# Kernel tuning notes

Measured on AMD Instinct MI355X. Metric: run time of the kernel, lower is better.

Reference implementation:

```python
import jax, jax.numpy as jnp
import numpy as np

B, N, FOV = 64, 128, 9
CH = [3, 32, 64, 128]
FLAT = CH[-1] * FOV * FOV  # 10368
ENC = 128
K = 3
G1, G2 = 128, 128
A = 5
EPS = 1e-5


def setup_inputs() -> dict:
    key = jax.random.key(0)
    ks = jax.random.split(key, 24)
    d = {}
    d["states"] = jax.random.normal(ks[0], (B, N, 3, FOV, FOV), jnp.float32)
    d["gso"] = jax.random.uniform(ks[1], (B, N, N), jnp.float32)
    i = 2
    for l in range(3):
        cin, cout = CH[l], CH[l + 1]
        d[f"c{l+1}_w"] = jax.random.normal(ks[i], (cout, cin, 3, 3), jnp.float32) * 0.05; i += 1
        d[f"c{l+1}_b"] = jnp.zeros((cout,), jnp.float32)
        d[f"c{l+1}_g"] = jnp.ones((cout,), jnp.float32)
        d[f"c{l+1}_be"] = jnp.zeros((cout,), jnp.float32)
    d["enc_w"] = jax.random.normal(ks[i], (ENC, FLAT), jnp.float32) * (1.0 / np.sqrt(FLAT)); i += 1
    d["enc_b"] = jnp.zeros((ENC,), jnp.float32)
    d["g1_w"] = jax.random.normal(ks[i], (K, G1, ENC), jnp.float32) * (1.0 / np.sqrt(ENC * K)); i += 1
    d["g1_b"] = jnp.zeros((G1,), jnp.float32)
    d["g2_w"] = jax.random.normal(ks[i], (K, G2, G1), jnp.float32) * (1.0 / np.sqrt(G1 * K)); i += 1
    d["g2_b"] = jnp.zeros((G2,), jnp.float32)
    d["act_w"] = jax.random.normal(ks[i], (A, G2), jnp.float32) * (1.0 / np.sqrt(G2)); i += 1
    d["act_b"] = jnp.zeros((A,), jnp.float32)
    return d


def _conv_bn_relu(x, w, b, gamma, beta):
    # 3x3, stride 1, padding 1 -> SAME; NCHW/OIHW
    y = jax.lax.conv_general_dilated(
        x, w, window_strides=(1, 1), padding="SAME",
        dimension_numbers=("NCHW", "OIHW", "NCHW"))
    y = y + b[None, :, None, None]
    # BatchNorm2d in training mode: batch statistics over (N, H, W)
    mu = jnp.mean(y, axis=(0, 2, 3), keepdims=True)
    var = jnp.var(y, axis=(0, 2, 3), keepdims=True)
    y = (y - mu) * jax.lax.rsqrt(var + EPS)
    y = y * gamma[None, :, None, None] + beta[None, :, None, None]
    return jax.nn.relu(y)


def _graph_filter(x, S, w, b):
    # x: [B, F, N], S: [B, N, N], w: [K, G, F] -> y = sum_k W_k (x S^k) + b
    out = jnp.einsum("bfn,gf->bgn", x, w[0])
    xk = x
    for k in range(1, w.shape[0]):
        xk = jnp.einsum("bfn,bnm->bfm", xk, S)
        out = out + jnp.einsum("bfn,gf->bgn", xk, w[k])
    return out + b[None, :, None]


def reference(states, gso,
              c1_w, c1_b, c1_g, c1_be,
              c2_w, c2_b, c2_g, c2_be,
              c3_w, c3_b, c3_g, c3_be,
              enc_w, enc_b, g1_w, g1_b, g2_w, g2_b, act_w, act_b):
    x = states.reshape(B * N, 3, FOV, FOV)
    x = _conv_bn_relu(x, c1_w, c1_b, c1_g, c1_be)
    x = _conv_bn_relu(x, c2_w, c2_b, c2_g, c2_be)
    x = _conv_bn_relu(x, c3_w, c3_b, c3_g, c3_be)
    x = x.reshape(B * N, FLAT)
    x = x @ enc_w.T + enc_b                    # [B*N, ENC]
    x = x.reshape(B, N, ENC).transpose(0, 2, 1)  # [B, F, N]
    x = jax.nn.relu(_graph_filter(x, gso, g1_w, g1_b))
    x = jax.nn.relu(_graph_filter(x, gso, g2_w, g2_b))
    x = x.transpose(0, 2, 1).reshape(B * N, G2)
    logits = x @ act_w.T + act_b
    return logits.reshape(B, N, A)
```

## Files before the change

### kernel.cpp

```cpp
#include <hip/hip_runtime.h>
#include <hip/hip_bf16.h>
#include <stdint.h>


#define NIMG 8192
#define NPIX 81
#define FLAT 10368

typedef __hip_bfloat16 bf16;
typedef short bf16x8 __attribute__((ext_vector_type(8)));
typedef float f32x4 __attribute__((ext_vector_type(4)));

__device__ __forceinline__ float bflo(unsigned u) { return __uint_as_float(u << 16); }
__device__ __forceinline__ float bfhi(unsigned u) { return __uint_as_float(u & 0xffff0000u); }
__device__ __forceinline__ unsigned short f2bf(float f) {
    unsigned u = __float_as_uint(f);
    return (unsigned short)((u + 0x7fff + ((u >> 16) & 1)) >> 16);
}

__device__ __forceinline__ bf16x8 bn8(bf16x8 a, const float* sc, const float* sh) {
    union U { bf16x8 v; unsigned u[4]; } in, out;
    in.v = a;
#pragma unroll
    for (int d = 0; d < 4; d++) {
        float lo = fmaxf(fmaf(bflo(in.u[d]), sc[2 * d],     sh[2 * d]),     0.f);
        float hi = fmaxf(fmaf(bfhi(in.u[d]), sc[2 * d + 1], sh[2 * d + 1]), 0.f);
        out.u[d] = (unsigned)f2bf(lo) | ((unsigned)f2bf(hi) << 16);
    }
    return out.v;
}

__global__ void fill_sentinel(float* __restrict__ out, int n) {
    int i = blockIdx.x * 256 + threadIdx.x;
    if (i < n) out[i] = 1.0e9f;
}

__global__ void prep_w(const float* __restrict__ c1w, const float* __restrict__ c2w,
                       const float* __restrict__ c3w,
                       float* __restrict__ w1t, bf16* __restrict__ w2m,
                       bf16* __restrict__ w3m) {
    int i0 = blockIdx.x * blockDim.x + threadIdx.x;
    int stride = gridDim.x * blockDim.x;
    for (int i = i0; i < 27 * 32; i += stride) w1t[i] = c1w[(i & 31) * 27 + (i >> 5)];
    for (int i = i0; i < 64 * 288; i += stride) {
        int oc = i / 288, r = i - oc * 288, t = r >> 5, ci = r & 31;
        w2m[i] = __float2bfloat16(c2w[oc * 288 + ci * 9 + t]);
    }
    for (int i = i0; i < 128 * 576; i += stride) {
        int oc = i / 576, r = i - oc * 576, t = r >> 6, ci = r & 63;
        w3m[i] = __float2bfloat16(c3w[oc * 576 + ci * 9 + t]);
    }
}

__global__ void prep_enc(const float* __restrict__ encw, bf16* __restrict__ ewb) {
    int i0 = blockIdx.x * blockDim.x + threadIdx.x;
    int stride = gridDim.x * blockDim.x;
    for (int i = i0; i < 128 * FLAT; i += stride) {
        int e = i / FLAT, r = i - e * FLAT;
        int kk = r >> 5, c32 = r & 31;
        int px = kk >> 2, cc = kk & 3;
        ewb[i] = __float2bfloat16(encw[(size_t)e * FLAT + (cc * 32 + c32) * 81 + px]);
    }
}

__device__ __forceinline__ void load_row(const float* __restrict__ p, float* r) {
    float4 a = *(const float4*)p;
    float4 b = *(const float4*)(p + 4);
    float4 c = *(const float4*)(p + 8);
    r[0]=a.x; r[1]=a.y; r[2]=a.z;  r[3]=a.w;
    r[4]=b.x; r[5]=b.y; r[6]=b.z;  r[7]=b.w;
    r[8]=c.x; r[9]=c.y; r[10]=c.z; r[11]=c.w;
}

__device__ __forceinline__ void conv_body(const float* __restrict__ inp,
                                          const float* __restrict__ wv, float* acc) {
    float rb[3][12];
    load_row(inp, rb[0]);
    load_row(inp + 12, rb[1]);
#pragma unroll
    for (int oy = 0; oy < 9; oy++) {
        load_row(inp + (oy + 2) * 12, rb[(oy + 2) % 3]);
#pragma unroll
        for (int ky = 0; ky < 3; ky++) {
            const float* r = rb[(oy + ky) % 3];
#pragma unroll
            for (int ox = 0; ox < 9; ox++) {
                float s = acc[oy * 9 + ox];
                s = fmaf(r[ox + 0], wv[ky * 3 + 0], s);
                s = fmaf(r[ox + 1], wv[ky * 3 + 1], s);
                s = fmaf(r[ox + 2], wv[ky * 3 + 2], s);
                acc[oy * 9 + ox] = s;
            }
        }
    }
}

__global__ __launch_bounds__(128) void conv1_kernel(const float* __restrict__ xin,
        const float* __restrict__ wt, const float* __restrict__ bias,
        bf16* __restrict__ xout, float* __restrict__ sacc) {
    __shared__ __align__(16) float lds[4 * 3 * 132];
    __shared__ float Sl[128], Ql[128];
    int t = threadIdx.x;
    int img0 = blockIdx.x * 4;
    for (int i = t; i < 4 * 3 * 132; i += 128) lds[i] = 0.f;
    __syncthreads();
    const float* src = xin + (size_t)img0 * 243;
    for (int i = t; i < 4 * 243; i += 128) {
        int il = i / 243, rem = i - il * 243;
        int ci = rem / 81, px = rem - ci * 81;
        lds[(il * 3 + ci) * 132 + (px / 9 + 1) * 12 + (px % 9) + 1] = src[i];
    }
    __syncthreads();
    int oc = t & 31, il = t >> 5;
    const float* base = lds + il * 3 * 132;
    float acc[81];
    float bb = bias[oc];
#pragma unroll
    for (int i = 0; i < 81; i++) acc[i] = bb;
#pragma unroll
    for (int ci = 0; ci < 3; ci++) {
        float wv[9];
#pragma unroll
        for (int k = 0; k < 9; k++) wv[k] = wt[(ci * 9 + k) * 32 + oc];
        conv_body(base + ci * 132, wv, acc);
    }
    bf16* dst = xout + (size_t)(img0 + il) * 32 + oc;
    const size_t PXS = (size_t)NIMG * 32;
    float s = 0.f, q = 0.f;
#pragma unroll
    for (int p = 0; p < 81; p++) {
        float v = acc[p];
        s += v; q = fmaf(v, v, q);
        dst[p * PXS] = __float2bfloat16(v);
    }
    Sl[il * 32 + oc] = s;
    Ql[il * 32 + oc] = q;
    __syncthreads();
    if (t < 32)
        atomicAdd(&sacc[t], Sl[t] + Sl[32 + t] + Sl[64 + t] + Sl[96 + t]);
    else if (t < 64) {
        int c = t - 32;
        atomicAdd(&sacc[32 + c], Ql[c] + Ql[32 + c] + Ql[64 + c] + Ql[96 + c]);
    }
}

template <int CI, int COT, int OCS>
__global__ __launch_bounds__(256, 2) void conv_tile(const bf16* __restrict__ xin,
        const bf16* __restrict__ wm, const float* __restrict__ bias,
        const float* __restrict__ st, bf16* __restrict__ xout,
        float* __restrict__ sacc) {
    constexpr int NCH = CI / 32;
    constexpr int NCHO = COT / 32;
    constexpr int ROW = 9 * CI;
    constexpr int STEPS = 9 * NCH;
    constexpr int PHASES = STEPS / 9;
    constexpr int HS = STEPS / PHASES;
    constexpr size_t CSTRIDE = (size_t)NIMG * 32;
    __shared__ bf16 Bs[HS * 4 * 64 * 8];
    __shared__ float Ss[2][4][64];

    const int lin = blockIdx.x;
    const int xcd = lin & 7;
    const int slot = lin >> 3;
    constexpr int PSL = 81 * OCS;
    const int igl = slot / PSL;
    const int rem = slot - igl * PSL;
    const int p = rem / OCS;
    const int ob = rem - p * OCS;
    const int ig = xcd * 4 + igl;
    const int oc0 = ob * 64;
    const int py = p / 9, pxx = p - py * 9;
    const int tid = threadIdx.x;
    const int lane = tid & 63, wv = tid >> 6;
    const int m = lane & 15, quad = lane >> 4;
    const long img0 = (long)ig * 256 + wv * 64;

    int qt[9]; bool vt[9];
#pragma unroll
    for (int t = 0; t < 9; t++) {
        int iy = py + t / 3 - 1, ix = pxx + (t % 3) - 1;
        vt[t] = ((unsigned)iy < 9u) && ((unsigned)ix < 9u);
        qt[t] = vt[t] ? iy * 9 + ix : p;
    }

    float scv[NCH][8], shv[NCH][8];
#pragma unroll
    for (int ch = 0; ch < NCH; ch++)
#pragma unroll
        for (int j = 0; j < 8; j++) {
            int ci = ch * 32 + quad * 8 + j;
            scv[ch][j] = st[ci];
            shv[ch][j] = st[CI + ci];
        }

    f32x4 acc[4][4];
#pragma unroll
    for (int nf = 0; nf < 4; nf++) {
        float bb = bias[oc0 + nf * 16 + m];
#pragma unroll
        for (int ms = 0; ms < 4; ms++) {
            acc[ms][nf][0] = bb; acc[ms][nf][1] = bb;
            acc[ms][nf][2] = bb; acc[ms][nf][3] = bb;
        }
    }
    const bf16* ab[4];
#pragma unroll
    for (int ms = 0; ms < 4; ms++)
        ab[ms] = xin + (img0 + ms * 16 + m) * 32 + quad * 8;

    const bf16* bsl = &Bs[lane * 8];
    const bf16x8 zf = {0, 0, 0, 0, 0, 0, 0, 0};

#pragma unroll
    for (int ph = 0; ph < PHASES; ph++) {
        __syncthreads();
        for (int i = tid; i < HS * 4 * 64; i += 256) {
            int l2 = i & 63, nf = (i >> 6) & 3, sl = i >> 8;
            int s = ph * HS + sl;
            int t = s / NCH, ch = s - t * NCH;
            int mm = l2 & 15, qq = l2 >> 4;
            *(bf16x8*)(&Bs[(size_t)i * 8]) =
                *(const bf16x8*)(wm + (size_t)(oc0 + nf * 16 + mm) * ROW + t * CI + ch * 32 + qq * 8);
        }
        __syncthreads();
#pragma unroll
        for (int sl = 0; sl < HS; sl++) {
            const int s = ph * HS + sl;
            const int t = s / NCH, ch = s - t * NCH;
            bf16x8 bfr[4];
#pragma unroll
            for (int nf = 0; nf < 4; nf++)
                bfr[nf] = *(const bf16x8*)(bsl + (sl * 4 + nf) * 512);
            bf16x8 a[4];
#pragma unroll
            for (int ms = 0; ms < 4; ms++)
                a[ms] = *(const bf16x8*)(ab[ms] + (size_t)(qt[t] * NCH + ch) * CSTRIDE);
#pragma unroll
            for (int ms = 0; ms < 4; ms++) {
                bf16x8 v = vt[t] ? bn8(a[ms], scv[ch], shv[ch]) : zf;
#pragma unroll
                for (int nf = 0; nf < 4; nf++)
                    acc[ms][nf] = __builtin_amdgcn_mfma_f32_16x16x32_bf16(v, bfr[nf], acc[ms][nf], 0, 0, 0);
            }
        }
    }

    const int och = oc0 >> 5;
#pragma unroll
    for (int ms = 0; ms < 4; ms++)
#pragma unroll
        for (int nf = 0; nf < 4; nf++) {
            bf16* orow = xout
                + (((size_t)p * NCHO + och + (nf >> 1)) * NIMG + img0 + ms * 16 + quad * 4) * 32
                + (nf & 1) * 16 + m;
#pragma unroll
            for (int r = 0; r < 4; r++)
                orow[r * 32] = __float2bfloat16(acc[ms][nf][r]);
        }

    float ssum[4], sq[4];
#pragma unroll
    for (int nf = 0; nf < 4; nf++) {
        float s = 0.f, q = 0.f;
#pragma unroll
        for (int ms = 0; ms < 4; ms++)
#pragma unroll
            for (int r = 0; r < 4; r++) {
                float v = acc[ms][nf][r];
                s += v; q = fmaf(v, v, q);
            }
        s += __shfl_xor(s, 16); s += __shfl_xor(s, 32);
        q += __shfl_xor(q, 16); q += __shfl_xor(q, 32);
        ssum[nf] = s; sq[nf] = q;
    }
    if (lane < 16) {
#pragma unroll
        for (int nf = 0; nf < 4; nf++) {
            Ss[0][wv][nf * 16 + lane] = ssum[nf];
            Ss[1][wv][nf * 16 + lane] = sq[nf];
        }
    }
    __syncthreads();
    if (tid < 64) {
        float a = Ss[0][0][tid] + Ss[0][1][tid] + Ss[0][2][tid] + Ss[0][3][tid];
        atomicAdd(&sacc[oc0 + tid], a);
    } else if (tid < 128) {
        int c = tid - 64;
        float a = Ss[1][0][c] + Ss[1][1][c] + Ss[1][2][c] + Ss[1][3][c];
        atomicAdd(&sacc[COT + oc0 + c], a);
    }
}

__global__ __launch_bounds__(256) void enc_mfma(const bf16* __restrict__ x3,
        const bf16* __restrict__ ewb, const float* __restrict__ st,
        float* __restrict__ part) {
    const int lin = blockIdx.x;
    const int xcd = lin & 7;
    const int slot = lin >> 3;
    const int igl = slot >> 3;
    const int combo = slot & 7;
    const int ks = combo >> 1, nh = combo & 1;
    const int ig = xcd * 8 + igl;
    const int lane = threadIdx.x & 63, wv = threadIdx.x >> 6;
    const int m = lane & 15, quad = lane >> 4;
    const long img0 = (long)ig * 128 + wv * 32;
    constexpr size_t CSTRIDE = (size_t)NIMG * 32;

    float scv[4][8], shv[4][8];
#pragma unroll
    for (int cc = 0; cc < 4; cc++)
#pragma unroll
        for (int j = 0; j < 8; j++) {
            int ci = cc * 32 + quad * 8 + j;
            scv[cc][j] = st[ci];
            shv[cc][j] = st[128 + ci];
        }

    f32x4 acc[2][4];
#pragma unroll
    for (int ms = 0; ms < 2; ms++)
#pragma unroll
        for (int nf = 0; nf < 4; nf++) {
            acc[ms][nf][0]=0.f; acc[ms][nf][1]=0.f; acc[ms][nf][2]=0.f; acc[ms][nf][3]=0.f;
        }
    const bf16* ab[2];
    const bf16* bb[4];
#pragma unroll
    for (int ms = 0; ms < 2; ms++)
        ab[ms] = x3 + (size_t)(ks * 81) * CSTRIDE + (img0 + ms * 16 + m) * 32 + quad * 8;
#pragma unroll
    for (int nf = 0; nf < 4; nf++)
        bb[nf] = ewb + (size_t)(nh * 64 + nf * 16 + m) * FLAT + ks * 81 * 32 + quad * 8;

#pragma unroll 3
    for (int c = 0; c < 81; c++) {
        const int cc = (ks + c) & 3;
        bf16x8 Ac[2], Bc[4];
#pragma unroll
        for (int ms = 0; ms < 2; ms++) {
            bf16x8 raw = *(const bf16x8*)(ab[ms] + (size_t)c * CSTRIDE);
            Ac[ms] = bn8(raw, scv[cc], shv[cc]);
        }
#pragma unroll
        for (int nf = 0; nf < 4; nf++) Bc[nf] = *(const bf16x8*)(bb[nf] + c * 32);
#pragma unroll
        for (int nf = 0; nf < 4; nf++)
#pragma unroll
            for (int ms = 0; ms < 2; ms++)
                acc[ms][nf] = __builtin_amdgcn_mfma_f32_16x16x32_bf16(Ac[ms], Bc[nf], acc[ms][nf], 0, 0, 0);
    }

    float* pp = part + (size_t)ks * (NIMG * 128) + (img0 + quad * 4) * 128 + nh * 64 + m;
#pragma unroll
    for (int ms = 0; ms < 2; ms++)
#pragma unroll
        for (int nf = 0; nf < 4; nf++)
#pragma unroll
            for (int r = 0; r < 4; r++)
                pp[(ms * 16 + r) * 128 + nf * 16] = acc[ms][nf][r];
}

template <int CO>
__global__ void stats_fin(const float* __restrict__ acc, const float* __restrict__ gamma,
                          const float* __restrict__ beta, float* __restrict__ st) {
    int c = threadIdx.x;
    if (c < CO) {
        const float inv = 1.0f / (8192.0f * 81.0f);
        float m = acc[c] * inv;
        float var = acc[CO + c] * inv - m * m;
        float istd = rsqrtf(var + 1e-5f);
        float sc = istd * gamma[c];
        st[c] = sc;
        st[CO + c] = beta[c] - m * sc;
    }
}

__global__ void enc_reduce(const float* __restrict__ part, const float* __restrict__ encb,
                           float* __restrict__ xT) {
    int i = blockIdx.x * 256 + threadIdx.x;
    const int NP = NIMG * 128;
    if (i < NP) {
        float v = part[i] + part[NP + i] + part[2 * NP + i] + part[3 * NP + i] + encb[i & 127];
        int img = i >> 7, f = i & 127;
        xT[(size_t)(img >> 7) * 16384 + f * 128 + (img & 127)] = v;
    }
}

__global__ __launch_bounds__(256) void mm_xs(const float* __restrict__ A,
        const float* __restrict__ S, float* __restrict__ Y) {
    __shared__ __align__(16) float Sc[32 * 132];
    __shared__ float Acm[32 * 33];
    int b = blockIdx.y, f0 = blockIdx.x * 32;
    int t = threadIdx.x;
    int fl = t & 31, mg = t >> 5;
    const float* Ab = A + (size_t)b * 16384;
    const float* Sb = S + (size_t)b * 16384;
    float acc[16];
#pragma unroll
    for (int j = 0; j < 16; j++) acc[j] = 0.f;
    for (int nc = 0; nc < 128; nc += 32) {
#pragma unroll
        for (int r = 0; r < 4; r++) {
            int i4 = r * 256 + t;
            int nn = i4 >> 5, m4 = (i4 & 31) * 4;
            *(float4*)&Sc[nn * 132 + m4] = *(const float4*)&Sb[(size_t)(nc + nn) * 128 + m4];
        }
#pragma unroll
        for (int r = 0; r < 4; r++) {
            int i = r * 256 + t;
            int ff = i >> 5, nn = i & 31;
            Acm[ff * 33 + nn] = Ab[(size_t)(f0 + ff) * 128 + nc + nn];
        }
        __syncthreads();
#pragma unroll 4
        for (int nn = 0; nn < 32; nn++) {
            float a = Acm[fl * 33 + nn];
#pragma unroll
            for (int j = 0; j < 4; j++) {
                float4 s4 = *(const float4*)&Sc[nn * 132 + mg * 16 + j * 4];
                acc[j*4+0] = fmaf(a, s4.x, acc[j*4+0]);
                acc[j*4+1] = fmaf(a, s4.y, acc[j*4+1]);
                acc[j*4+2] = fmaf(a, s4.z, acc[j*4+2]);
                acc[j*4+3] = fmaf(a, s4.w, acc[j*4+3]);
            }
        }
        __syncthreads();
    }
    float* yb = Y + (size_t)b * 16384 + (size_t)(f0 + fl) * 128 + mg * 16;
#pragma unroll
    for (int j = 0; j < 4; j++)
        *(float4*)&yb[j * 4] = make_float4(acc[j*4], acc[j*4+1], acc[j*4+2], acc[j*4+3]);
}

__global__ __launch_bounds__(256) void gf_combine(const float* __restrict__ Z0,
        const float* __restrict__ Z1, const float* __restrict__ Z2,
        const float* __restrict__ W, const float* __restrict__ bias,
        float* __restrict__ out) {
    __shared__ __align__(16) float Zc[32 * 132];
    __shared__ float Wc[32 * 33];
    int b = blockIdx.y, g0 = blockIdx.x * 32;
    int t = threadIdx.x;
    int gl = t & 31, mg = t >> 5;
    float acc[16];
    float bb = bias[g0 + gl];
#pragma unroll
    for (int j = 0; j < 16; j++) acc[j] = bb;
    const float* Zs[3] = {Z0 + (size_t)b * 16384, Z1 + (size_t)b * 16384, Z2 + (size_t)b * 16384};
    for (int j3 = 0; j3 < 3; j3++) {
        const float* Zb = Zs[j3];
        const float* Wj = W + j3 * 16384;
        for (int fc = 0; fc < 128; fc += 32) {
#pragma unroll
            for (int r = 0; r < 4; r++) {
                int i4 = r * 256 + t;
                int ff = i4 >> 5, m4 = (i4 & 31) * 4;
                *(float4*)&Zc[ff * 132 + m4] = *(const float4*)&Zb[(size_t)(fc + ff) * 128 + m4];
            }
#pragma unroll
            for (int r = 0; r < 4; r++) {
                int i = r * 256 + t;
                int gg = i >> 5, ff = i & 31;
                Wc[gg * 33 + ff] = Wj[(size_t)(g0 + gg) * 128 + fc + ff];
            }
            __syncthreads();
#pragma unroll 4
            for (int ff = 0; ff < 32; ff++) {
                float w = Wc[gl * 33 + ff];
#pragma unroll
                for (int j = 0; j < 4; j++) {
                    float4 z4 = *(const float4*)&Zc[ff * 132 + mg * 16 + j * 4];
                    acc[j*4+0] = fmaf(w, z4.x, acc[j*4+0]);
                    acc[j*4+1] = fmaf(w, z4.y, acc[j*4+1]);
                    acc[j*4+2] = fmaf(w, z4.z, acc[j*4+2]);
                    acc[j*4+3] = fmaf(w, z4.w, acc[j*4+3]);
                }
            }
            __syncthreads();
        }
    }
    float* ob = out + (size_t)b * 16384 + (size_t)(g0 + gl) * 128 + mg * 16;
#pragma unroll
    for (int j = 0; j < 4; j++)
        *(float4*)&ob[j * 4] = make_float4(fmaxf(acc[j*4], 0.f), fmaxf(acc[j*4+1], 0.f),
                                           fmaxf(acc[j*4+2], 0.f), fmaxf(acc[j*4+3], 0.f));
}

__global__ __launch_bounds__(128) void act_kernel(const float* __restrict__ X,
        const float* __restrict__ aw, const float* __restrict__ ab,
        float* __restrict__ out) {
    int b = blockIdx.x, n = threadIdx.x;
    float acc[5];
#pragma unroll
    for (int a = 0; a < 5; a++) acc[a] = ab[a];
    const float* xb = X + (size_t)b * 16384 + n;
#pragma unroll 4
    for (int g = 0; g < 128; g++) {
        float v = xb[(size_t)g * 128];
#pragma unroll
        for (int a = 0; a < 5; a++) acc[a] = fmaf(v, aw[a * 128 + g], acc[a]);
    }
    float* ob = out + ((size_t)b * 128 + n) * 5;
#pragma unroll
    for (int a = 0; a < 5; a++) ob[a] = acc[a];
}

extern "C" void kernel_launch(void* const* d_in, const int* in_sizes, int n_in,
                              void* d_out, int out_size, void* d_ws, size_t ws_size,
                              hipStream_t stream) {
    const float* states = (const float*)d_in[0];
    const float* gso    = (const float*)d_in[1];
    const float* c1w  = (const float*)d_in[2];
    const float* c1b  = (const float*)d_in[3];
    const float* c1g  = (const float*)d_in[4];
    const float* c1be = (const float*)d_in[5];
    const float* c2w  = (const float*)d_in[6];
    const float* c2b  = (const float*)d_in[7];
    const float* c2g  = (const float*)d_in[8];
    const float* c2be = (const float*)d_in[9];
    const float* c3w  = (const float*)d_in[10];
    const float* c3b  = (const float*)d_in[11];
    const float* c3g  = (const float*)d_in[12];
    const float* c3be = (const float*)d_in[13];
    const float* encw = (const float*)d_in[14];
    const float* encb = (const float*)d_in[15];
    const float* g1w  = (const float*)d_in[16];
    const float* g1b  = (const float*)d_in[17];
    const float* g2w  = (const float*)d_in[18];
    const float* g2b  = (const float*)d_in[19];
    const float* aw   = (const float*)d_in[20];
    const float* ab   = (const float*)d_in[21];
    float* out = (float*)d_out;
    char* ws = (char*)d_ws;

    size_t o = 0;
    auto take = [&](size_t bytes) { size_t r = o; o += (bytes + 255) & ~(size_t)255; return r; };
    const size_t o_x3  = take((size_t)81 * 4 * NIMG * 32 * 2);
    const size_t o_x2  = take((size_t)81 * 2 * NIMG * 32 * 2);
    const size_t o_w1t = take(27 * 32 * 4);
    const size_t o_w2m = take(64 * 288 * 2);
    const size_t o_w3m = take(128 * 576 * 2);
    const size_t o_acc = take(448 * 4);
    const size_t o_st1 = take(2 * 32 * 4);
    const size_t o_st2 = take(2 * 64 * 4);
    const size_t o_st3 = take(2 * 128 * 4);
    if (ws_size < o) {
        fill_sentinel<<<(out_size + 255) / 256, 256, 0, stream>>>(out, out_size);
        return;
    }

    const size_t o_x1 = o_x3;
    const size_t o_ewb  = o_x2;
    const size_t o_part = o_x2 + 2654208;
    const size_t o_xT   = o_part + 16777216;
    const size_t o_y1   = o_xT + 4194304;
    const size_t o_y2   = o_y1 + 4194304;
    const size_t o_G1   = o_y2 + 4194304;
    const size_t o_G2   = o_G1 + 4194304;

    bf16* x1 = (bf16*)(ws + o_x1);
    bf16* x2 = (bf16*)(ws + o_x2);
    bf16* x3 = (bf16*)(ws + o_x3);
    float* w1t = (float*)(ws + o_w1t);
    bf16* w2m = (bf16*)(ws + o_w2m);
    bf16* w3m = (bf16*)(ws + o_w3m);
    float* acc1 = (float*)(ws + o_acc);
    float* acc2 = acc1 + 64;
    float* acc3 = acc1 + 192;
    float* st1 = (float*)(ws + o_st1);
    float* st2 = (float*)(ws + o_st2);
    float* st3 = (float*)(ws + o_st3);
    bf16* ewb = (bf16*)(ws + o_ewb);
    float* partp = (float*)(ws + o_part);
    float* xT = (float*)(ws + o_xT);
    float* y1 = (float*)(ws + o_y1);
    float* y2 = (float*)(ws + o_y2);
    float* xG1 = (float*)(ws + o_G1);
    float* xG2 = (float*)(ws + o_G2);

    hipMemsetAsync(ws + o_acc, 0, 448 * 4, stream);
    prep_w<<<128, 256, 0, stream>>>(c1w, c2w, c3w, w1t, w2m, w3m);

    conv1_kernel<<<2048, 128, 0, stream>>>(states, w1t, c1b, x1, acc1);
    stats_fin<32><<<1, 32, 0, stream>>>(acc1, c1g, c1be, st1);

    conv_tile<32, 64, 1><<<2592, 256, 0, stream>>>(x1, w2m, c2b, st1, x2, acc2);
    stats_fin<64><<<1, 64, 0, stream>>>(acc2, c2g, c2be, st2);

    conv_tile<64, 128, 2><<<5184, 256, 0, stream>>>(x2, w3m, c3b, st2, x3, acc3);
    stats_fin<128><<<1, 128, 0, stream>>>(acc3, c3g, c3be, st3);

    prep_enc<<<2048, 256, 0, stream>>>(encw, ewb);
    enc_mfma<<<512, 256, 0, stream>>>(x3, ewb, st3, partp);
    enc_reduce<<<4096, 256, 0, stream>>>(partp, encb, xT);

    mm_xs<<<dim3(4, 64), 256, 0, stream>>>(xT, gso, y1);
    mm_xs<<<dim3(4, 64), 256, 0, stream>>>(y1, gso, y2);
    gf_combine<<<dim3(4, 64), 256, 0, stream>>>(xT, y1, y2, g1w, g1b, xG1);

    mm_xs<<<dim3(4, 64), 256, 0, stream>>>(xG1, gso, y1);
    mm_xs<<<dim3(4, 64), 256, 0, stream>>>(y1, gso, y2);
    gf_combine<<<dim3(4, 64), 256, 0, stream>>>(xG1, y1, y2, g2w, g2b, xG2);

    act_kernel<<<64, 128, 0, stream>>>(xG2, aw, ab, out);
}
```

Baseline: 751.0 us.

## Hoist BN+ReLU out of conv tiles into separate in-place pass; skip padded taps

Batch-norm scale/shift plus ReLU used to be applied to every input fragment inside the conv MFMA loops. It now runs once per element in a separate in-place kernel after each stats finalisation. The conv kernels skip out-of-bounds taps entirely instead of feeding zeros, and raise launch-bounds occupancy from 2 to 4. This removes redundant per-tap BN arithmetic (each input was normalised up to 9 times) and the registers it used, at the cost of an extra read-write pass over the activations.

Result: faster. 700.0 us (-6.8%).

```diff
diff --git a/kernel.cpp b/kernel.cpp
--- a/kernel.cpp
+++ b/kernel.cpp
@@ -60,6 +60,26 @@
         int kk = r >> 5, c32 = r & 31;
         int px = kk >> 2, cc = kk & 3;
         ewb[i] = __float2bfloat16(encw[(size_t)e * FLAT + (cc * 32 + c32) * 81 + px]);
+    }
+}
+
+template <int NCH>
+__global__ __launch_bounds__(256) void bnrelu_k(bf16* __restrict__ x,
+        const float* __restrict__ st, int n8) {
+    int i0 = blockIdx.x * 256 + threadIdx.x;
+    int stride = gridDim.x * 256;
+    for (int i = i0; i < n8; i += stride) {
+        size_t base = (size_t)i * 8;
+        int ch = (int)((base >> 18) & (unsigned)(NCH - 1));
+        int c0 = ch * 32 + (int)(base & 31);
+        float sc[8], sh[8];
+#pragma unroll
+        for (int j = 0; j < 8; j++) {
+            sc[j] = st[c0 + j];
+            sh[j] = st[NCH * 32 + c0 + j];
+        }
+        bf16x8 v = *(bf16x8*)(x + base);
+        *(bf16x8*)(x + base) = bn8(v, sc, sh);
     }
 }
 
@@ -145,10 +165,9 @@
 }
 
 template <int CI, int COT, int OCS>
-__global__ __launch_bounds__(256, 2) void conv_tile(const bf16* __restrict__ xin,
+__global__ __launch_bounds__(256, 4) void conv_tile(const bf16* __restrict__ xin,
         const bf16* __restrict__ wm, const float* __restrict__ bias,
-        const float* __restrict__ st, bf16* __restrict__ xout,
-        float* __restrict__ sacc) {
+        bf16* __restrict__ xout, float* __restrict__ sacc) {
     constexpr int NCH = CI / 32;
     constexpr int NCHO = COT / 32;
     constexpr int ROW = 9 * CI;
@@ -183,16 +202,6 @@
         qt[t] = vt[t] ? iy * 9 + ix : p;
     }
 
-    float scv[NCH][8], shv[NCH][8];
-#pragma unroll
-    for (int ch = 0; ch < NCH; ch++)
-#pragma unroll
-        for (int j = 0; j < 8; j++) {
-            int ci = ch * 32 + quad * 8 + j;
-            scv[ch][j] = st[ci];
-            shv[ch][j] = st[CI + ci];
-        }
-
     f32x4 acc[4][4];
 #pragma unroll
     for (int nf = 0; nf < 4; nf++) {
@@ -209,7 +218,6 @@
         ab[ms] = xin + (img0 + ms * 16 + m) * 32 + quad * 8;
 
     const bf16* bsl = &Bs[lane * 8];
-    const bf16x8 zf = {0, 0, 0, 0, 0, 0, 0, 0};
 
 #pragma unroll
     for (int ph = 0; ph < PHASES; ph++) {
@@ -227,20 +235,21 @@
         for (int sl = 0; sl < HS; sl++) {
             const int s = ph * HS + sl;
             const int t = s / NCH, ch = s - t * NCH;
-            bf16x8 bfr[4];
-#pragma unroll
-            for (int nf = 0; nf < 4; nf++)
-                bfr[nf] = *(const bf16x8*)(bsl + (sl * 4 + nf) * 512);
-            bf16x8 a[4];
-#pragma unroll
-            for (int ms = 0; ms < 4; ms++)
-                a[ms] = *(const bf16x8*)(ab[ms] + (size_t)(qt[t] * NCH + ch) * CSTRIDE);
-#pragma unroll
-            for (int ms = 0; ms < 4; ms++) {
-                bf16x8 v = vt[t] ? bn8(a[ms], scv[ch], shv[ch]) : zf;
+            if (vt[t]) {
+                bf16x8 bfr[4];
 #pragma unroll
                 for (int nf = 0; nf < 4; nf++)
-                    acc[ms][nf] = __builtin_amdgcn_mfma_f32_16x16x32_bf16(v, bfr[nf], acc[ms][nf], 0, 0, 0);
+                    bfr[nf] = *(const bf16x8*)(bsl + (sl * 4 + nf) * 512);
+                bf16x8 a[4];
+#pragma unroll
+                for (int ms = 0; ms < 4; ms++)
+                    a[ms] = *(const bf16x8*)(ab[ms] + (size_t)(qt[t] * NCH + ch) * CSTRIDE);
+#pragma unroll
+                for (int ms = 0; ms < 4; ms++) {
+#pragma unroll
+                    for (int nf = 0; nf < 4; nf++)
+                        acc[ms][nf] = __builtin_amdgcn_mfma_f32_16x16x32_bf16(a[ms], bfr[nf], acc[ms][nf], 0, 0, 0);
+                }
             }
         }
     }
@@ -582,11 +591,13 @@
 
     conv1_kernel<<<2048, 128, 0, stream>>>(states, w1t, c1b, x1, acc1);
     stats_fin<32><<<1, 32, 0, stream>>>(acc1, c1g, c1be, st1);
-
-    conv_tile<32, 64, 1><<<2592, 256, 0, stream>>>(x1, w2m, c2b, st1, x2, acc2);
+    bnrelu_k<1><<<4096, 256, 0, stream>>>(x1, st1, 81 * 1 * NIMG * 32 / 8);
+
+    conv_tile<32, 64, 1><<<2592, 256, 0, stream>>>(x1, w2m, c2b, x2, acc2);
     stats_fin<64><<<1, 64, 0, stream>>>(acc2, c2g, c2be, st2);
-
-    conv_tile<64, 128, 2><<<5184, 256, 0, stream>>>(x2, w3m, c3b, st2, x3, acc3);
+    bnrelu_k<2><<<4096, 256, 0, stream>>>(x2, st2, 81 * 2 * NIMG * 32 / 8);
+
+    conv_tile<64, 128, 2><<<5184, 256, 0, stream>>>(x2, w3m, c3b, x3, acc3);
     stats_fin<128><<<1, 128, 0, stream>>>(acc3, c3g, c3be, st3);
 
     prep_enc<<<2048, 256, 0, stream>>>(encw, ewb);
```
